# Performance work log

Hardware: AMD Instinct MI355X
Metric: run time of the kernel (lower is better)

The kernel has to match this reference:

```python
import jax, jax.numpy as jnp
import numpy as np

N = 100000   # nodes
E = 3200000  # directed edges
IN = 128     # in_channels
H = 16       # hidden_channels
OUT = 2      # out_channels
EPS = 1e-5   # BatchNorm eps


def setup_inputs() -> dict:
    key = jax.random.key(0)
    ks = jax.random.split(key, 16)
    x = jax.random.normal(ks[0], (N, IN), jnp.float32)
    edge_index = jax.random.randint(ks[1], (2, E), 0, N, jnp.int32)

    def lin(k, fan_in, fan_out):
        return jax.random.normal(k, (fan_in, fan_out), jnp.float32) / np.sqrt(fan_in)

    return {
        "x": x,
        "edge_index": edge_index,
        "W1": lin(ks[2], IN, H), "b1": jnp.zeros((H,), jnp.float32),
        "W2": lin(ks[3], H, H), "b2": jnp.zeros((H,), jnp.float32),
        "W3": lin(ks[4], H, H), "b3": jnp.zeros((H,), jnp.float32),
        "gamma1": jnp.ones((H,), jnp.float32), "beta1": jnp.zeros((H,), jnp.float32),
        "gamma2": jnp.ones((H,), jnp.float32), "beta2": jnp.zeros((H,), jnp.float32),
        "Wfc": lin(ks[5], H, OUT), "bfc": jnp.zeros((OUT,), jnp.float32),
    }


def reference(x, edge_index, W1, b1, W2, b2, W3, b3,
              gamma1, beta1, gamma2, beta2, Wfc, bfc):
    src, dst = edge_index[0], edge_index[1]
    # symmetric GCN normalization with self loops: deg includes +1 self loop
    deg = jax.ops.segment_sum(jnp.ones((E,), x.dtype), dst, num_segments=N) + 1.0
    dis = jax.lax.rsqrt(deg)                      # [N]
    norm = dis[src] * dis[dst]                    # [E]

    def gcn_conv(h, W, b):
        hw = h @ W                                # [N, F] dense transform
        msg = norm[:, None] * hw[src]             # gather + scale  [E, F]
        agg = jax.ops.segment_sum(msg, dst, num_segments=N)
        agg = agg + (dis * dis)[:, None] * hw     # self-loop contribution
        return agg + b

    def batch_norm(h, g, be):
        mu = h.mean(axis=0)
        var = h.var(axis=0)
        return (h - mu) * jax.lax.rsqrt(var + EPS) * g + be

    h = batch_norm(jax.nn.relu(gcn_conv(x, W1, b1)), gamma1, beta1)
    # dropout is identity in inference / deterministic reference
    h = batch_norm(jax.nn.relu(gcn_conv(h, W2, b2)), gamma2, beta2)
    h = gcn_conv(h, W3, b3)
    return jax.nn.log_softmax(h @ Wfc + bfc, axis=1)
```

## Files before the change

### kernel.cpp

```cpp
#include <hip/hip_runtime.h>
#include <hip/hip_fp16.h>

#define NN 100000
#define EE 3200000
#define INC 128
#define HC 16
#define BN_EPS 1e-5f

#define NPB 256
#define NBUCK ((NN + NPB - 1) / NPB)
#define CAPU 13440
#define BINSZ ((size_t)(NBUCK + 1) * CAPU)
#define BTILE 4096
#define BGRID ((EE + BTILE - 1) / BTILE)
#define SB_CAP 12288

#define XSTR 132

__device__ __forceinline__ __half2 bits_to_h2(int v) { __half2 h; *(int*)&h = v; return h; }
__device__ __forceinline__ int h2_to_bits(__half2 h) { return *(int*)&h; }


__global__ void init_cursor(int* __restrict__ bcursor) {
    int k = blockIdx.x * blockDim.x + threadIdx.x;
    if (k < NBUCK) bcursor[k] = k * CAPU;
}


__global__ __launch_bounds__(512) void bin_edges(const int* __restrict__ src,
                          const int* __restrict__ dst,
                          int* __restrict__ bcursor, unsigned* __restrict__ bin) {
    __shared__ unsigned stage[BTILE];
    __shared__ unsigned short sbuck[BTILE];
    __shared__ int hist[NBUCK], loff[NBUCK], gbase[NBUCK];
    __shared__ int wsum[8];
    int tid = threadIdx.x;
    int lane = tid & 63, wid = tid >> 6;
    for (int k = tid; k < NBUCK; k += 512) hist[k] = 0;
    __syncthreads();
    int e0 = blockIdx.x * BTILE;
    int cnt = min(BTILE, EE - e0);
    int n4 = cnt >> 2;
    const int4* d4 = (const int4*)(dst + e0);
    const int4* s4 = (const int4*)(src + e0);
    int4 dv0 = {0,0,0,0}, dv1 = {0,0,0,0}, sv0 = {0,0,0,0}, sv1 = {0,0,0,0};
    bool va0 = tid < n4, va1 = tid + 512 < n4;
    if (va0) {
        dv0 = d4[tid]; sv0 = s4[tid];
        atomicAdd(&hist[dv0.x >> 8], 1);
        atomicAdd(&hist[dv0.y >> 8], 1);
        atomicAdd(&hist[dv0.z >> 8], 1);
        atomicAdd(&hist[dv0.w >> 8], 1);
    }
    if (va1) {
        dv1 = d4[tid + 512]; sv1 = s4[tid + 512];
        atomicAdd(&hist[dv1.x >> 8], 1);
        atomicAdd(&hist[dv1.y >> 8], 1);
        atomicAdd(&hist[dv1.z >> 8], 1);
        atomicAdd(&hist[dv1.w >> 8], 1);
    }
    __syncthreads();
    int hv = (tid < NBUCK) ? hist[tid] : 0;
    int v = hv;
#pragma unroll
    for (int off = 1; off < 64; off <<= 1) {
        int t = __shfl_up(v, off);
        if (lane >= off) v += t;
    }
    if (lane == 63) wsum[wid] = v;
    __syncthreads();
    if (tid == 0) {
        int run = 0;
#pragma unroll
        for (int j = 0; j < 8; ++j) { int t = wsum[j]; wsum[j] = run; run += t; }
    }
    __syncthreads();
    int excl = v - hv + wsum[wid];
    if (tid < NBUCK) {
        loff[tid] = excl;
        if (hv) gbase[tid] = atomicAdd(&bcursor[tid], hv);
        hist[tid] = 0;
    }
    __syncthreads();
    {
        int d, s, k, p;
        if (va0) {
            d = dv0.x; s = sv0.x; k = d >> 8; p = loff[k] + atomicAdd(&hist[k], 1);
            stage[p] = ((unsigned)(d & 255) << 24) | (unsigned)s; sbuck[p] = (unsigned short)k;
            d = dv0.y; s = sv0.y; k = d >> 8; p = loff[k] + atomicAdd(&hist[k], 1);
            stage[p] = ((unsigned)(d & 255) << 24) | (unsigned)s; sbuck[p] = (unsigned short)k;
            d = dv0.z; s = sv0.z; k = d >> 8; p = loff[k] + atomicAdd(&hist[k], 1);
            stage[p] = ((unsigned)(d & 255) << 24) | (unsigned)s; sbuck[p] = (unsigned short)k;
            d = dv0.w; s = sv0.w; k = d >> 8; p = loff[k] + atomicAdd(&hist[k], 1);
            stage[p] = ((unsigned)(d & 255) << 24) | (unsigned)s; sbuck[p] = (unsigned short)k;
        }
        if (va1) {
            d = dv1.x; s = sv1.x; k = d >> 8; p = loff[k] + atomicAdd(&hist[k], 1);
            stage[p] = ((unsigned)(d & 255) << 24) | (unsigned)s; sbuck[p] = (unsigned short)k;
            d = dv1.y; s = sv1.y; k = d >> 8; p = loff[k] + atomicAdd(&hist[k], 1);
            stage[p] = ((unsigned)(d & 255) << 24) | (unsigned)s; sbuck[p] = (unsigned short)k;
            d = dv1.z; s = sv1.z; k = d >> 8; p = loff[k] + atomicAdd(&hist[k], 1);
            stage[p] = ((unsigned)(d & 255) << 24) | (unsigned)s; sbuck[p] = (unsigned short)k;
            d = dv1.w; s = sv1.w; k = d >> 8; p = loff[k] + atomicAdd(&hist[k], 1);
            stage[p] = ((unsigned)(d & 255) << 24) | (unsigned)s; sbuck[p] = (unsigned short)k;
        }
    }
    __syncthreads();
    for (int i = tid; i < cnt; i += 512) {
        int k = sbuck[i];
        int idx = gbase[k] + (i - loff[k]);
        if (idx < k * CAPU + SB_CAP) bin[idx] = stage[i];
    }
}


__global__ __launch_bounds__(512) void sort_bucket(const int* __restrict__ bcursor,
                            unsigned* __restrict__ bin,
                            unsigned* __restrict__ rowpack, float* __restrict__ dis) {
    __shared__ unsigned stg[SB_CAP];
    __shared__ int cnt[NPB], pos[NPB], sc[NPB];
    __shared__ int ptot_tot;
    int tid = threadIdx.x;
    for (int k = tid; k < NPB; k += 512) cnt[k] = 0;
    __syncthreads();
    int b = blockIdx.x;
    int beg = b * CAPU;
    int n = min(bcursor[b] - beg, SB_CAP);
    for (int i = tid; i < n; i += 512) {
        unsigned u = bin[beg + i];
        stg[i] = u;
        atomicAdd(&cnt[u >> 24], 1);
    }
    __syncthreads();
    int node = b * NPB + tid;
    int tot = 0, ptot = 0;
    if (tid < NPB) {
        tot = cnt[tid] + ((node < NN) ? 1 : 0);
        ptot = ((tot + 47) / 48) * 48;
        sc[tid] = ptot;
    }
    __syncthreads();
    for (int off = 1; off < NPB; off <<= 1) {
        int t = 0;
        if (tid < NPB && tid >= off) t = sc[tid - off];
        __syncthreads();
        if (tid < NPB) sc[tid] += t;
        __syncthreads();
    }
    int lo = 0;
    if (tid < NPB) {
        lo = sc[tid] - ptot;
        pos[tid] = lo + ((node < NN) ? 1 : 0);
        if (tid == NPB - 1) ptot_tot = sc[tid];
        if (node < NN) {
            rowpack[node] = ((unsigned)min(tot, 511) << 23) | (unsigned)(beg + lo);
            dis[node] = rsqrtf((float)tot);
        }
    }
    __syncthreads();
    unsigned padv = (unsigned)NN << 5;
    int fillN = ptot_tot;
    for (int i = tid; i < fillN; i += 512) bin[beg + i] = padv;
    __syncthreads();
    if (tid < NPB && node < NN) bin[beg + lo] = (unsigned)node << 5;
    for (int i = tid; i < n; i += 512) {
        unsigned u = stg[i];
        int nl = u >> 24;
        int p = atomicAdd(&pos[nl], 1);
        bin[beg + p] = (u & 0xFFFFFFu) << 5;
    }
}


__global__ void gemm_x_w1(const float* __restrict__ x, const float* __restrict__ W1,
                          const float* __restrict__ dis, __half2* __restrict__ hws2) {
    __shared__ float Ws[INC * HC];
    __shared__ float xs[16 * XSTR];
    int tid = threadIdx.x;
    for (int i = tid; i < INC * HC; i += 256) Ws[i] = W1[i];
    int node0 = blockIdx.x * 16;
    const float4* xsrc = (const float4*)(x + (size_t)node0 * INC);
    float4* xdst = (float4*)xs;
    int nvalid = min(16, NN - node0);
    int nf4 = nvalid * 32;
    for (int i = tid; i < nf4; i += 256) {
        int nl = i >> 5, k4 = i & 31;
        xdst[nl * 33 + k4] = xsrc[i];
    }
    __syncthreads();
    int c = tid & 15;
    int nl = tid >> 4;
    int node = node0 + nl;
    if (node >= NN) return;
    const float* xr = xs + nl * XSTR;
    float sum = 0.f;
#pragma unroll
    for (int k = 0; k < INC; ++k) sum += xr[k] * Ws[k * 16 + c];
    sum *= dis[node];
    float other = __shfl_xor(sum, 1);
    if ((c & 1) == 0) hws2[node * 8 + (c >> 1)] = __floats2half2_rn(sum, other);
}

__global__ void gemm_bn_h_w(const float* __restrict__ agg, const float* __restrict__ stats,
                            const float* __restrict__ gamma, const float* __restrict__ beta,
                            const float* __restrict__ W, const float* __restrict__ dis,
                            __half2* __restrict__ hws2) {
    __shared__ float Ws[HC * HC];
    __shared__ float sc[HC], sf[HC];
    int tid = threadIdx.x;
    if (tid < HC * HC) Ws[tid] = W[tid];
    if (tid < HC) {
        const float invN = 1.0f / NN;
        float mu = stats[tid] * invN;
        float var = stats[16 + tid] * invN - mu * mu;
        float rs = rsqrtf(var + BN_EPS);
        sc[tid] = gamma[tid] * rs;
        sf[tid] = beta[tid] - mu * gamma[tid] * rs;
    }
    __syncthreads();
    int i = blockIdx.x * 256 + tid;
    if (i >= NN * HC) return;
    int n = i >> 4, c = i & 15;
    const float4* ar = (const float4*)(agg + n * HC);
    float sum = 0.f;
#pragma unroll
    for (int q = 0; q < 4; ++q) {
        float4 v = ar[q];
        int k = q * 4;
        float h0 = fmaxf(v.x, 0.f) * sc[k + 0] + sf[k + 0];
        float h1 = fmaxf(v.y, 0.f) * sc[k + 1] + sf[k + 1];
        float h2 = fmaxf(v.z, 0.f) * sc[k + 2] + sf[k + 2];
        float h3 = fmaxf(v.w, 0.f) * sc[k + 3] + sf[k + 3];
        sum += h0 * Ws[(k + 0) * 16 + c] + h1 * Ws[(k + 1) * 16 + c]
             + h2 * Ws[(k + 2) * 16 + c] + h3 * Ws[(k + 3) * 16 + c];
    }
    sum *= dis[n];
    float other = __shfl_xor(sum, 1);
    if ((c & 1) == 0) hws2[n * 8 + (c >> 1)] = __floats2half2_rn(sum, other);
}


__global__ void gcn_gather(const unsigned* __restrict__ rowpack,
                           const unsigned* __restrict__ bin,
                           const __half2* __restrict__ hws2,
                           const float* __restrict__ b, float* __restrict__ agg) {
    int tid = threadIdx.x;
    int lane = tid & 63;
    int node = blockIdx.x * 4 + (tid >> 6);
    if (node >= NN) return;
    int cq = lane & 3;
    int slot = lane >> 2;
    unsigned rp = rowpack[node];
    int beg = (int)(rp & 0x7FFFFFu);
    int tot = (int)(rp >> 23);
    const char* hbase = (const char*)hws2;
    int e0 = beg + slot;
    unsigned v0 = bin[e0], v1 = bin[e0 + 16], v2 = bin[e0 + 32];
    int2 h0 = *(const int2*)(hbase + (size_t)v0 + cq * 8);
    int2 h1 = *(const int2*)(hbase + (size_t)v1 + cq * 8);
    int2 h2 = *(const int2*)(hbase + (size_t)v2 + cq * 8);
    __half2 accA = __hadd2(__hadd2(bits_to_h2(h0.x), bits_to_h2(h1.x)), bits_to_h2(h2.x));
    __half2 accB = __hadd2(__hadd2(bits_to_h2(h0.y), bits_to_h2(h1.y)), bits_to_h2(h2.y));
    for (int off = 48; off < tot; off += 48) {
        unsigned w0 = bin[e0 + off], w1 = bin[e0 + off + 16], w2 = bin[e0 + off + 32];
        int2 g0 = *(const int2*)(hbase + (size_t)w0 + cq * 8);
        int2 g1 = *(const int2*)(hbase + (size_t)w1 + cq * 8);
        int2 g2 = *(const int2*)(hbase + (size_t)w2 + cq * 8);
        accA = __hadd2(accA, __hadd2(__hadd2(bits_to_h2(g0.x), bits_to_h2(g1.x)), bits_to_h2(g2.x)));
        accB = __hadd2(accB, __hadd2(__hadd2(bits_to_h2(g0.y), bits_to_h2(g1.y)), bits_to_h2(g2.y)));
    }
    int ia = h2_to_bits(accA), ib = h2_to_bits(accB);
#pragma unroll
    for (int d = 4; d < 64; d <<= 1) {
        int oa = __shfl_xor(ia, d), ob = __shfl_xor(ib, d);
        accA = __hadd2(accA, bits_to_h2(oa));
        accB = __hadd2(accB, bits_to_h2(ob));
        ia = h2_to_bits(accA); ib = h2_to_bits(accB);
    }
    if (slot == 0) {
        float d = rsqrtf((float)tot);
        float2 sa = __half22float2(accA), sb = __half22float2(accB);
        float4 r;
        r.x = d * sa.x + b[4 * cq + 0];
        r.y = d * sa.y + b[4 * cq + 1];
        r.z = d * sb.x + b[4 * cq + 2];
        r.w = d * sb.y + b[4 * cq + 3];
        ((float4*)agg)[node * 4 + cq] = r;
    }
}

__global__ void gather_fc(const unsigned* __restrict__ rowpack,
                          const unsigned* __restrict__ bin,
                          const __half2* __restrict__ hws2,
                          const float* __restrict__ b, const float* __restrict__ Wfc,
                          const float* __restrict__ bfc, float* __restrict__ out) {
    int tid = threadIdx.x;
    int lane = tid & 63;
    int node = blockIdx.x * 4 + (tid >> 6);
    if (node >= NN) return;
    int cq = lane & 3;
    int slot = lane >> 2;
    unsigned rp = rowpack[node];
    int beg = (int)(rp & 0x7FFFFFu);
    int tot = (int)(rp >> 23);
    const char* hbase = (const char*)hws2;
    int e0 = beg + slot;
    unsigned v0 = bin[e0], v1 = bin[e0 + 16], v2 = bin[e0 + 32];
    int2 h0 = *(const int2*)(hbase + (size_t)v0 + cq * 8);
    int2 h1 = *(const int2*)(hbase + (size_t)v1 + cq * 8);
    int2 h2 = *(const int2*)(hbase + (size_t)v2 + cq * 8);
    __half2 accA = __hadd2(__hadd2(bits_to_h2(h0.x), bits_to_h2(h1.x)), bits_to_h2(h2.x));
    __half2 accB = __hadd2(__hadd2(bits_to_h2(h0.y), bits_to_h2(h1.y)), bits_to_h2(h2.y));
    for (int off = 48; off < tot; off += 48) {
        unsigned w0 = bin[e0 + off], w1 = bin[e0 + off + 16], w2 = bin[e0 + off + 32];
        int2 g0 = *(const int2*)(hbase + (size_t)w0 + cq * 8);
        int2 g1 = *(const int2*)(hbase + (size_t)w1 + cq * 8);
        int2 g2 = *(const int2*)(hbase + (size_t)w2 + cq * 8);
        accA = __hadd2(accA, __hadd2(__hadd2(bits_to_h2(g0.x), bits_to_h2(g1.x)), bits_to_h2(g2.x)));
        accB = __hadd2(accB, __hadd2(__hadd2(bits_to_h2(g0.y), bits_to_h2(g1.y)), bits_to_h2(g2.y)));
    }
    int ia = h2_to_bits(accA), ib = h2_to_bits(accB);
#pragma unroll
    for (int d = 4; d < 64; d <<= 1) {
        int oa = __shfl_xor(ia, d), ob = __shfl_xor(ib, d);
        accA = __hadd2(accA, bits_to_h2(oa));
        accB = __hadd2(accB, bits_to_h2(ob));
        ia = h2_to_bits(accA); ib = h2_to_bits(accB);
    }
    float z0 = 0.f, z1 = 0.f;
    if (slot == 0) {
        float d = rsqrtf((float)tot);
        float2 sa = __half22float2(accA), sb = __half22float2(accB);
        float v0f = d * sa.x + b[4 * cq + 0];
        float v1f = d * sa.y + b[4 * cq + 1];
        float v2f = d * sb.x + b[4 * cq + 2];
        float v3f = d * sb.y + b[4 * cq + 3];
        int k = 4 * cq;
        z0 = v0f * Wfc[(k + 0) * 2 + 0] + v1f * Wfc[(k + 1) * 2 + 0]
           + v2f * Wfc[(k + 2) * 2 + 0] + v3f * Wfc[(k + 3) * 2 + 0];
        z1 = v0f * Wfc[(k + 0) * 2 + 1] + v1f * Wfc[(k + 1) * 2 + 1]
           + v2f * Wfc[(k + 2) * 2 + 1] + v3f * Wfc[(k + 3) * 2 + 1];
    }
    z0 += __shfl_xor(z0, 1); z1 += __shfl_xor(z1, 1);
    z0 += __shfl_xor(z0, 2); z1 += __shfl_xor(z1, 2);
    if (lane == 0) {
        z0 += bfc[0]; z1 += bfc[1];
        float m = fmaxf(z0, z1);
        float lse = m + logf(expf(z0 - m) + expf(z1 - m));
        out[node * 2 + 0] = z0 - lse;
        out[node * 2 + 1] = z1 - lse;
    }
}


__global__ void bn_stats_final(const float* __restrict__ agg, float* __restrict__ stats) {
    int tid = threadIdx.x;
    float s0 = 0.f, s1 = 0.f, s2 = 0.f, s3 = 0.f;
    float q0 = 0.f, q1 = 0.f, q2 = 0.f, q3 = 0.f;
    const float4* a4 = (const float4*)agg;
    const int n4 = NN * HC / 4;
    int i0 = blockIdx.x * 256 + tid;
    for (int i = i0; i < n4; i += gridDim.x * 256) {
        float4 v = a4[i];
        float r0 = fmaxf(v.x, 0.f), r1 = fmaxf(v.y, 0.f);
        float r2 = fmaxf(v.z, 0.f), r3 = fmaxf(v.w, 0.f);
        s0 += r0; s1 += r1; s2 += r2; s3 += r3;
        q0 += r0 * r0; q1 += r1 * r1; q2 += r2 * r2; q3 += r3 * r3;
    }
    int quad = i0 & 3;
    __shared__ float acc[32];
    if (tid < 32) acc[tid] = 0.f;
    __syncthreads();
    atomicAdd(&acc[4 * quad + 0], s0);
    atomicAdd(&acc[4 * quad + 1], s1);
    atomicAdd(&acc[4 * quad + 2], s2);
    atomicAdd(&acc[4 * quad + 3], s3);
    atomicAdd(&acc[16 + 4 * quad + 0], q0);
    atomicAdd(&acc[16 + 4 * quad + 1], q1);
    atomicAdd(&acc[16 + 4 * quad + 2], q2);
    atomicAdd(&acc[16 + 4 * quad + 3], q3);
    __syncthreads();
    if (tid < 32) atomicAdd(&stats[tid], acc[tid]);
}


extern "C" void kernel_launch(void* const* d_in, const int* in_sizes, int n_in,
                              void* d_out, int out_size, void* d_ws, size_t ws_size,
                              hipStream_t stream) {
    const float* x    = (const float*)d_in[0];
    const int*   ei   = (const int*)d_in[1];
    const int*   src  = ei;
    const int*   dstp = ei + EE;
    const float* W1   = (const float*)d_in[2];
    const float* b1   = (const float*)d_in[3];
    const float* W2   = (const float*)d_in[4];
    const float* b2   = (const float*)d_in[5];
    const float* W3   = (const float*)d_in[6];
    const float* b3   = (const float*)d_in[7];
    const float* g1   = (const float*)d_in[8];
    const float* be1  = (const float*)d_in[9];
    const float* g2   = (const float*)d_in[10];
    const float* be2  = (const float*)d_in[11];
    const float* Wfc  = (const float*)d_in[12];
    const float* bfc  = (const float*)d_in[13];
    float* out = (float*)d_out;

    char* p = (char*)d_ws;
    unsigned* bin   = (unsigned*)p;             p += BINSZ * 4;
    __half2* hws2   = (__half2*)p;              p += (size_t)(NN + 1) * HC * 2;
    float*  agg     = (float*)p;                p += (size_t)NN * HC * 4;
    float*  dis     = (float*)p;                p += (size_t)NN * 4;
    unsigned* rowpack=(unsigned*)p;             p += (size_t)NN * 4;
    int*    bcursor = (int*)p;                  p += NBUCK * 4;
    float*  stats1  = (float*)p;                p += 32 * 4;
    float*  stats2  = (float*)p;                p += 32 * 4;

    const int TB = 256;
    const int gNH = (NN * HC + TB - 1) / TB;
    const int gX  = (NN + 15) / 16;
    const int gG  = (NN + 3) / 4;

    init_cursor<<<2, 256, 0, stream>>>(bcursor);
    hipMemsetAsync(stats1, 0, 64 * sizeof(float), stream);
    hipMemsetAsync(hws2 + (size_t)NN * 8, 0, HC * 2, stream);
    bin_edges<<<BGRID, 512, 0, stream>>>(src, dstp, bcursor, bin);
    sort_bucket<<<NBUCK, 512, 0, stream>>>(bcursor, bin, rowpack, dis);

    gemm_x_w1<<<gX, TB, 0, stream>>>(x, W1, dis, hws2);
    gcn_gather<<<gG, TB, 0, stream>>>(rowpack, bin, hws2, b1, agg);
    bn_stats_final<<<1024, TB, 0, stream>>>(agg, stats1);

    gemm_bn_h_w<<<gNH, TB, 0, stream>>>(agg, stats1, g1, be1, W2, dis, hws2);
    gcn_gather<<<gG, TB, 0, stream>>>(rowpack, bin, hws2, b2, agg);
    bn_stats_final<<<1024, TB, 0, stream>>>(agg, stats2);

    gemm_bn_h_w<<<gNH, TB, 0, stream>>>(agg, stats2, g2, be2, W3, dis, hws2);
    gather_fc<<<gG, TB, 0, stream>>>(rowpack, bin, hws2, b3, Wfc, bfc, out);
}
```

Measured before the change: 255.7 us.

## Fuse W1 GEMM into binning launch and BN statistics into gather

Runs the x@W1 transform as extra blocks of the edge-binning kernel, writing unscaled fp16 features that sort_bucket then scales by the degree norm once it is known. Gather kernels now apply ReLU, store the activated values, and emit per-block BN sum and sum-of-squares partials. A small reduce kernel combines those partials, replacing the full re-read of agg in bn_stats_final. Gather blocks grow to 8 nodes each and bounds checks are dropped on the assumption that NN divides evenly. The cost is an extra hw_raw buffer, extra fp16 rounding of the scaled features, and one added read and write of the features in sort_bucket.

```diff
diff --git a/kernel.cpp b/kernel.cpp
--- a/kernel.cpp
+++ b/kernel.cpp
@@ -14,6 +14,8 @@
 #define BTILE 4096
 #define BGRID ((EE + BTILE - 1) / BTILE)
 #define SB_CAP 12288
+#define GX32 (NN / 32)
+#define GGRID (NN / 8)
 
 #define XSTR 132
 
@@ -27,14 +29,39 @@
 }
 
 
-__global__ __launch_bounds__(512) void bin_edges(const int* __restrict__ src,
+__global__ __launch_bounds__(512) void build_gemm(const int* __restrict__ src,
                           const int* __restrict__ dst,
-                          int* __restrict__ bcursor, unsigned* __restrict__ bin) {
+                          int* __restrict__ bcursor, unsigned* __restrict__ bin,
+                          const float* __restrict__ x, const float* __restrict__ W1,
+                          __half2* __restrict__ hw_raw) {
     __shared__ unsigned stage[BTILE];
     __shared__ unsigned short sbuck[BTILE];
     __shared__ int hist[NBUCK], loff[NBUCK], gbase[NBUCK];
     __shared__ int wsum[8];
-    int tid = threadIdx.x;
+    __shared__ float Ws[INC * HC];
+    __shared__ float xs[32 * XSTR];
+    int tid = threadIdx.x;
+    if (blockIdx.x >= BGRID) {
+        for (int i = tid; i < INC * HC; i += 512) Ws[i] = W1[i];
+        int node0 = (blockIdx.x - BGRID) * 32;
+        const float4* xsrc = (const float4*)(x + (size_t)node0 * INC);
+        float4* xdst = (float4*)xs;
+        for (int i = tid; i < 1024; i += 512) {
+            int nl = i >> 5, k4 = i & 31;
+            xdst[nl * 33 + k4] = xsrc[i];
+        }
+        __syncthreads();
+        int c = tid & 15;
+        int nl = tid >> 4;
+        int node = node0 + nl;
+        const float* xr = xs + nl * XSTR;
+        float sum = 0.f;
+#pragma unroll
+        for (int k = 0; k < INC; ++k) sum += xr[k] * Ws[k * 16 + c];
+        float other = __shfl_xor(sum, 1);
+        if ((c & 1) == 0) hw_raw[node * 8 + (c >> 1)] = __floats2half2_rn(sum, other);
+        return;
+    }
     int lane = tid & 63, wid = tid >> 6;
     for (int k = tid; k < NBUCK; k += 512) hist[k] = 0;
     __syncthreads();
@@ -116,7 +143,8 @@
 
 __global__ __launch_bounds__(512) void sort_bucket(const int* __restrict__ bcursor,
                             unsigned* __restrict__ bin,
-                            unsigned* __restrict__ rowpack, float* __restrict__ dis) {
+                            unsigned* __restrict__ rowpack, float* __restrict__ dis,
+                            const __half2* __restrict__ hw_raw, __half2* __restrict__ hws2) {
     __shared__ unsigned stg[SB_CAP];
     __shared__ int cnt[NPB], pos[NPB], sc[NPB];
     __shared__ int ptot_tot;
@@ -154,7 +182,16 @@
         if (tid == NPB - 1) ptot_tot = sc[tid];
         if (node < NN) {
             rowpack[node] = ((unsigned)min(tot, 511) << 23) | (unsigned)(beg + lo);
-            dis[node] = rsqrtf((float)tot);
+            float dv = rsqrtf((float)tot);
+            dis[node] = dv;
+            __half2 d2 = __float2half2_rn(dv);
+            const int4* hr = (const int4*)(hw_raw + (size_t)node * 8);
+            int4 a = hr[0], bq = hr[1];
+            __half2* ha = (__half2*)&a; __half2* hb = (__half2*)&bq;
+#pragma unroll
+            for (int j = 0; j < 4; ++j) { ha[j] = __hmul2(ha[j], d2); hb[j] = __hmul2(hb[j], d2); }
+            int4* hw = (int4*)(hws2 + (size_t)node * 8);
+            hw[0] = a; hw[1] = bq;
         }
     }
     __syncthreads();
@@ -171,35 +208,6 @@
     }
 }
 
-
-__global__ void gemm_x_w1(const float* __restrict__ x, const float* __restrict__ W1,
-                          const float* __restrict__ dis, __half2* __restrict__ hws2) {
-    __shared__ float Ws[INC * HC];
-    __shared__ float xs[16 * XSTR];
-    int tid = threadIdx.x;
-    for (int i = tid; i < INC * HC; i += 256) Ws[i] = W1[i];
-    int node0 = blockIdx.x * 16;
-    const float4* xsrc = (const float4*)(x + (size_t)node0 * INC);
-    float4* xdst = (float4*)xs;
-    int nvalid = min(16, NN - node0);
-    int nf4 = nvalid * 32;
-    for (int i = tid; i < nf4; i += 256) {
-        int nl = i >> 5, k4 = i & 31;
-        xdst[nl * 33 + k4] = xsrc[i];
-    }
-    __syncthreads();
-    int c = tid & 15;
-    int nl = tid >> 4;
-    int node = node0 + nl;
-    if (node >= NN) return;
-    const float* xr = xs + nl * XSTR;
-    float sum = 0.f;
-#pragma unroll
-    for (int k = 0; k < INC; ++k) sum += xr[k] * Ws[k * 16 + c];
-    sum *= dis[node];
-    float other = __shfl_xor(sum, 1);
-    if ((c & 1) == 0) hws2[node * 8 + (c >> 1)] = __floats2half2_rn(sum, other);
-}
 
 __global__ void gemm_bn_h_w(const float* __restrict__ agg, const float* __restrict__ stats,
                             const float* __restrict__ gamma, const float* __restrict__ beta,
@@ -227,10 +235,10 @@
     for (int q = 0; q < 4; ++q) {
         float4 v = ar[q];
         int k = q * 4;
-        float h0 = fmaxf(v.x, 0.f) * sc[k + 0] + sf[k + 0];
-        float h1 = fmaxf(v.y, 0.f) * sc[k + 1] + sf[k + 1];
-        float h2 = fmaxf(v.z, 0.f) * sc[k + 2] + sf[k + 2];
-        float h3 = fmaxf(v.w, 0.f) * sc[k + 3] + sf[k + 3];
+        float h0 = v.x * sc[k + 0] + sf[k + 0];
+        float h1 = v.y * sc[k + 1] + sf[k + 1];
+        float h2 = v.z * sc[k + 2] + sf[k + 2];
+        float h3 = v.w * sc[k + 3] + sf[k + 3];
         sum += h0 * Ws[(k + 0) * 16 + c] + h1 * Ws[(k + 1) * 16 + c]
              + h2 * Ws[(k + 2) * 16 + c] + h3 * Ws[(k + 3) * 16 + c];
     }
@@ -240,14 +248,17 @@
 }
 
 
-__global__ void gcn_gather(const unsigned* __restrict__ rowpack,
+__global__ __launch_bounds__(512) void gcn_gather(const unsigned* __restrict__ rowpack,
                            const unsigned* __restrict__ bin,
                            const __half2* __restrict__ hws2,
-                           const float* __restrict__ b, float* __restrict__ agg) {
-    int tid = threadIdx.x;
+                           const float* __restrict__ b, float* __restrict__ agg,
+                           float* __restrict__ partials) {
+    __shared__ float acc[32];
+    int tid = threadIdx.x;
+    if (tid < 32) acc[tid] = 0.f;
+    __syncthreads();
     int lane = tid & 63;
-    int node = blockIdx.x * 4 + (tid >> 6);
-    if (node >= NN) return;
+    int node = blockIdx.x * 8 + (tid >> 6);
     int cq = lane & 3;
     int slot = lane >> 2;
     unsigned rp = rowpack[node];
@@ -280,24 +291,49 @@
     if (slot == 0) {
         float d = rsqrtf((float)tot);
         float2 sa = __half22float2(accA), sb = __half22float2(accB);
-        float4 r;
-        r.x = d * sa.x + b[4 * cq + 0];
-        r.y = d * sa.y + b[4 * cq + 1];
-        r.z = d * sb.x + b[4 * cq + 2];
-        r.w = d * sb.y + b[4 * cq + 3];
+        float t0 = fmaxf(d * sa.x + b[4 * cq + 0], 0.f);
+        float t1 = fmaxf(d * sa.y + b[4 * cq + 1], 0.f);
+        float t2 = fmaxf(d * sb.x + b[4 * cq + 2], 0.f);
+        float t3 = fmaxf(d * sb.y + b[4 * cq + 3], 0.f);
+        float4 r; r.x = t0; r.y = t1; r.z = t2; r.w = t3;
         ((float4*)agg)[node * 4 + cq] = r;
-    }
-}
-
-__global__ void gather_fc(const unsigned* __restrict__ rowpack,
+        atomicAdd(&acc[4 * cq + 0], t0);
+        atomicAdd(&acc[4 * cq + 1], t1);
+        atomicAdd(&acc[4 * cq + 2], t2);
+        atomicAdd(&acc[4 * cq + 3], t3);
+        atomicAdd(&acc[16 + 4 * cq + 0], t0 * t0);
+        atomicAdd(&acc[16 + 4 * cq + 1], t1 * t1);
+        atomicAdd(&acc[16 + 4 * cq + 2], t2 * t2);
+        atomicAdd(&acc[16 + 4 * cq + 3], t3 * t3);
+    }
+    __syncthreads();
+    if (tid < 32) partials[(size_t)blockIdx.x * 32 + tid] = acc[tid];
+}
+
+
+__global__ void reduce_stats(const float* __restrict__ partials, float* __restrict__ stats) {
+    int tid = threadIdx.x;
+    const int total = GGRID * 32;
+    float a = 0.f;
+    int i0 = blockIdx.x * 256 + tid;
+    for (int i = i0; i < total; i += gridDim.x * 256) a += partials[i];
+    __shared__ float acc[32];
+    if (tid < 32) acc[tid] = 0.f;
+    __syncthreads();
+    atomicAdd(&acc[i0 & 31], a);
+    __syncthreads();
+    if (tid < 32) atomicAdd(&stats[tid], acc[tid]);
+}
+
+
+__global__ __launch_bounds__(512) void gather_fc(const unsigned* __restrict__ rowpack,
                           const unsigned* __restrict__ bin,
                           const __half2* __restrict__ hws2,
                           const float* __restrict__ b, const float* __restrict__ Wfc,
                           const float* __restrict__ bfc, float* __restrict__ out) {
     int tid = threadIdx.x;
     int lane = tid & 63;
-    int node = blockIdx.x * 4 + (tid >> 6);
-    if (node >= NN) return;
+    int node = blockIdx.x * 8 + (tid >> 6);
     int cq = lane & 3;
     int slot = lane >> 2;
     unsigned rp = rowpack[node];
@@ -353,37 +389,6 @@
 }
 
 
-__global__ void bn_stats_final(const float* __restrict__ agg, float* __restrict__ stats) {
-    int tid = threadIdx.x;
-    float s0 = 0.f, s1 = 0.f, s2 = 0.f, s3 = 0.f;
-    float q0 = 0.f, q1 = 0.f, q2 = 0.f, q3 = 0.f;
-    const float4* a4 = (const float4*)agg;
-    const int n4 = NN * HC / 4;
-    int i0 = blockIdx.x * 256 + tid;
-    for (int i = i0; i < n4; i += gridDim.x * 256) {
-        float4 v = a4[i];
-        float r0 = fmaxf(v.x, 0.f), r1 = fmaxf(v.y, 0.f);
-        float r2 = fmaxf(v.z, 0.f), r3 = fmaxf(v.w, 0.f);
-        s0 += r0; s1 += r1; s2 += r2; s3 += r3;
-        q0 += r0 * r0; q1 += r1 * r1; q2 += r2 * r2; q3 += r3 * r3;
-    }
-    int quad = i0 & 3;
-    __shared__ float acc[32];
-    if (tid < 32) acc[tid] = 0.f;
-    __syncthreads();
-    atomicAdd(&acc[4 * quad + 0], s0);
-    atomicAdd(&acc[4 * quad + 1], s1);
-    atomicAdd(&acc[4 * quad + 2], s2);
-    atomicAdd(&acc[4 * quad + 3], s3);
-    atomicAdd(&acc[16 + 4 * quad + 0], q0);
-    atomicAdd(&acc[16 + 4 * quad + 1], q1);
-    atomicAdd(&acc[16 + 4 * quad + 2], q2);
-    atomicAdd(&acc[16 + 4 * quad + 3], q3);
-    __syncthreads();
-    if (tid < 32) atomicAdd(&stats[tid], acc[tid]);
-}
-
-
 extern "C" void kernel_launch(void* const* d_in, const int* in_sizes, int n_in,
                               void* d_out, int out_size, void* d_ws, size_t ws_size,
                               hipStream_t stream) {
@@ -408,32 +413,31 @@
     char* p = (char*)d_ws;
     unsigned* bin   = (unsigned*)p;             p += BINSZ * 4;
     __half2* hws2   = (__half2*)p;              p += (size_t)(NN + 1) * HC * 2;
+    __half2* hw_raw = (__half2*)p;              p += (size_t)NN * HC * 2;
     float*  agg     = (float*)p;                p += (size_t)NN * HC * 4;
     float*  dis     = (float*)p;                p += (size_t)NN * 4;
     unsigned* rowpack=(unsigned*)p;             p += (size_t)NN * 4;
+    float*  partials= (float*)p;                p += (size_t)GGRID * 32 * 4;
     int*    bcursor = (int*)p;                  p += NBUCK * 4;
     float*  stats1  = (float*)p;                p += 32 * 4;
     float*  stats2  = (float*)p;                p += 32 * 4;
 
     const int TB = 256;
     const int gNH = (NN * HC + TB - 1) / TB;
-    const int gX  = (NN + 15) / 16;
-    const int gG  = (NN + 3) / 4;
 
     init_cursor<<<2, 256, 0, stream>>>(bcursor);
     hipMemsetAsync(stats1, 0, 64 * sizeof(float), stream);
     hipMemsetAsync(hws2 + (size_t)NN * 8, 0, HC * 2, stream);
-    bin_edges<<<BGRID, 512, 0, stream>>>(src, dstp, bcursor, bin);
-    sort_bucket<<<NBUCK, 512, 0, stream>>>(bcursor, bin, rowpack, dis);
-
-    gemm_x_w1<<<gX, TB, 0, stream>>>(x, W1, dis, hws2);
-    gcn_gather<<<gG, TB, 0, stream>>>(rowpack, bin, hws2, b1, agg);
-    bn_stats_final<<<1024, TB, 0, stream>>>(agg, stats1);
+    build_gemm<<<BGRID + GX32, 512, 0, stream>>>(src, dstp, bcursor, bin, x, W1, hw_raw);
+    sort_bucket<<<NBUCK, 512, 0, stream>>>(bcursor, bin, rowpack, dis, hw_raw, hws2);
+
+    gcn_gather<<<GGRID, 512, 0, stream>>>(rowpack, bin, hws2, b1, agg, partials);
+    reduce_stats<<<64, 256, 0, stream>>>(partials, stats1);
 
     gemm_bn_h_w<<<gNH, TB, 0, stream>>>(agg, stats1, g1, be1, W2, dis, hws2);
-    gcn_gather<<<gG, TB, 0, stream>>>(rowpack, bin, hws2, b2, agg);
-    bn_stats_final<<<1024, TB, 0, stream>>>(agg, stats2);
+    gcn_gather<<<GGRID, 512, 0, stream>>>(rowpack, bin, hws2, b2, agg, partials);
+    reduce_stats<<<64, 256, 0, stream>>>(partials, stats2);
 
     gemm_bn_h_w<<<gNH, TB, 0, stream>>>(agg, stats2, g2, be2, W3, dis, hws2);
-    gather_fc<<<gG, TB, 0, stream>>>(rowpack, bin, hws2, b3, Wfc, bfc, out);
-}
+    gather_fc<<<GGRID, 512, 0, stream>>>(rowpack, bin, hws2, b3, Wfc, bfc, out);
+}
```

Result: faster. 240.2 us (-6.1%).
